# Kernel tuning notes

Hardware: AMD Instinct MI355X
Metric: run time of the kernel (lower is better)

## Reference

```python
import jax, jax.numpy as jnp
import numpy as np

PI = 3.1415927410125732
N = 4096
L = 1.28e-3          # box side [m]
VEL = 5e-7
RC = 3.15e-6         # Rc = diameter/2
RR = 8e-6
RO = 2.5e-5
RA = np.inf
DT_TRANS = 1.4e-14   # DT (translational diffusion)
DR = 0.0028
GAMMA = 25.0
DT = 0.2             # timestep dt
COLL_ITERS = 30      # fixed cap for collision-resolution do-while (orig caps at 1000)


def setup_inputs() -> dict:
    key = jax.random.key(0)
    ks = jax.random.split(key, 7)
    pos_re = jax.random.uniform(ks[0], (N,), jnp.float32) * L
    pos_im = jax.random.uniform(ks[1], (N,), jnp.float32) * L
    ang = jax.random.uniform(ks[2], (N,), jnp.float32, -PI, PI)
    ori_re = jnp.cos(ang)
    ori_im = jnp.sin(ang)
    deltas = jax.random.uniform(ks[3], (N,), jnp.float32) * 0.5
    rot_noise = jax.random.normal(ks[4], (N,), jnp.float32)
    tn_re = jax.random.normal(ks[5], (N,), jnp.float32)
    tn_im = jax.random.normal(ks[6], (N,), jnp.float32)
    return {"pos_re": pos_re, "pos_im": pos_im, "ori_re": ori_re, "ori_im": ori_im,
            "deltas": deltas, "rot_noise": rot_noise, "tn_re": tn_re, "tn_im": tn_im}


def _wrap(diff):
    # torch get_anglediff wrap: (-2pi,2pi) -> ~(-pi,pi)
    diff = jnp.where(diff <= -PI, jnp.mod(diff, PI), diff)
    return diff - (diff >= PI).astype(diff.dtype) * (2.0 * PI)


def _anglediff(a, b):
    return _wrap(jnp.angle(a) - jnp.angle(b))


def _cossim(a, b):
    # nn.CosineSimilarity(dim=1, eps=1e-14) on view_as_real vectors
    dot = a.real * b.real + a.imag * b.imag
    na = jnp.maximum(jnp.abs(a), 1e-14)
    nb = jnp.maximum(jnp.abs(b), 1e-14)
    return dot / (na * nb)


def _mvc(W, z):
    # real [n,n] mask @ complex [n] vector
    return W @ z.real + 1j * (W @ z.imag)


def _solve_collisions(pos):
    n = pos.shape[0]
    eye_f = jnp.eye(n, dtype=jnp.float32)
    eye_c = eye_f.astype(pos.dtype)

    def step(p):
        diff = p[None, :] - p[:, None] + eye_c  # [i,j] = pos_j - pos_i; diag dummy 1 (nan-safe)
        absd = jnp.abs(diff)
        coll = absd <= (2.0 * RC - eye_f)       # diag threshold negative -> self excluded
        move = jnp.where(coll, diff / jnp.where(coll, absd, 1.0) * ((2.1 * RC - absd) * 0.5), 0.0)
        return p - move.sum(axis=1), coll.sum()

    def body(carry, _):
        p, cont = carry
        p_new, ncoll = step(p)
        p = jnp.where(cont, p_new, p)           # do-while: apply move, then continue if collisions
        return (p, jnp.logical_and(cont, ncoll > 0)), None

    body = jax.checkpoint(body)
    (pos, _), _ = jax.lax.scan(body, (pos, jnp.array(True)), None, length=COLL_ITERS)
    return pos


def _forward(pos_re, pos_im, ori_re, ori_im, deltas, rot_noise, tn_re, tn_im):
    pos = (pos_re + 1j * pos_im).astype(jnp.complex64)
    ori = (ori_re + 1j * ori_im).astype(jnp.complex64)
    n = pos.shape[0]
    eye_b = jnp.eye(n, dtype=bool)

    # pairwise |pos_i - pos_j|; diag made 1 to keep abs() grad-safe (diag is masked out / re-added below)
    dists = jnp.abs(pos[:, None] - pos[None, :] + jnp.eye(n, dtype=pos.dtype))
    mask_rr = (dists <= RR) & ~eye_b              # repulsion zone, self excluded (eye subtracted in orig)
    mask_ro = (dists <= RO + RC) | eye_b          # orientation zone, self included (diag dist 0 in orig)
    mask_ra = (dists <= RA + RC) | eye_b          # Ra = inf -> all ones

    # alpha == 2*pi exactly -> within_view branch skipped (matches original)
    ang = jnp.angle(ori)
    abs_ad = jnp.abs(_wrap(ang[:, None] - ang[None, :]))
    in_front = abs_ad < PI / 2

    Wrr = (mask_rr & in_front).astype(jnp.float32)
    Wro = mask_ro.astype(jnp.float32)
    Wra = mask_ra.astype(jnp.float32)

    n_r = Wrr.sum(axis=1)
    S = _mvc(Wrr, pos) / jnp.maximum(n_r, 1.0) - pos * jnp.sign(n_r)
    d = -S

    n_a = Wra.sum(axis=1)
    cms = _mvc(Wra, pos) / jnp.maximum(n_a, 1.0)
    Ps = cms - pos * jnp.sign(n_a)

    osum = _mvc(Wro, ori)
    left = Ps * jnp.exp(1j * deltas)
    right = Ps * jnp.exp(-1j * deltas)

    # T (=300) >= T_release (=200): choose best turn by cosine similarity
    best = jnp.where(_cossim(left, osum) >= _cossim(right, osum), left, right)

    has_rep = jnp.abs(d) > 0.0
    d_safe = jnp.where(has_rep, d, jnp.ones_like(d))
    att = jnp.where(has_rep, _anglediff(d_safe, ori), _anglediff(best, ori))

    s2dr = np.float32(np.sqrt(2.0 * DR))
    sdt = np.float32(np.sqrt(DT))
    rot = jnp.exp(1j * (DT * GAMMA * DR * jnp.sin(att) + rot_noise * s2dr * sdt))

    # complex standard normal: real/imag each N(0, 1/sqrt(2))
    tnoise = (tn_re + 1j * tn_im) * np.float32(np.sqrt(0.5)) * np.float32(np.sqrt(2.0 * DT_TRANS))
    trans = DT * VEL * ori + tnoise * sdt

    new_pos = _solve_collisions(pos + trans)
    new_ori = ori * rot

    c2r = lambda z: jnp.stack([z.real, z.imag], axis=-1)
    # [5, N, 2]: positions, orientations, orientation_sums, leftturns, rightturns (real views)
    return jnp.stack([c2r(new_pos), c2r(new_ori), c2r(osum), c2r(left), c2r(right)], axis=0)


def reference(pos_re, pos_im, ori_re, ori_im, deltas, rot_noise, tn_re, tn_im):
    return _forward(pos_re, pos_im, ori_re, ori_im, deltas, rot_noise, tn_re, tn_im)
```

## Files before the change

### kernel.cpp

```cpp
#include <hip/hip_runtime.h>

#define NPART 4096
#define PI_F 3.1415927410125732f
#define TWO_PI_F 6.2831854820251465f
#define NBCAP 14336
#define SENT 4096

__device__ __forceinline__ float wrapf(float d) {
    if (d <= -PI_F) {
        d = fmodf(d, PI_F);
        if (d < 0.0f) d += PI_F;
    }
    if (d >= PI_F) d -= TWO_PI_F;
    return d;
}

__global__ __launch_bounds__(512)
void k_interact(const float* __restrict__ pr, const float* __restrict__ pim,
                const float* __restrict__ orr, const float* __restrict__ oim,
                const float* __restrict__ deltas,
                const float* __restrict__ rot_noise,
                const float* __restrict__ tn_re, const float* __restrict__ tn_im,
                float* __restrict__ out,
                float2* __restrict__ recPos, int* __restrict__ recMeta,
                unsigned short* __restrict__ recNbr, int* __restrict__ gcnt) {
    constexpr float RR_F  = 8e-6f;
    constexpr float RR2   = RR_F * RR_F;
    constexpr float ROC_F = (float)(2.5e-5 + 3.15e-6);
    constexpr float ROC2  = ROC_F * ROC_F;
    constexpr float CUT_F = 14.3e-6f;
    constexpr float CUT2  = CUT_F * CUT_F;

    __shared__ float4 ls4[512];
    __shared__ float red0[512], red1[512], red2[512], red3[512], red4[512];
    __shared__ float cr_[512], ci_[512];
    __shared__ int ncnt[8];
    __shared__ unsigned short nbrL[8 * 16];

    int tid = threadIdx.x;
    int li = tid & 7, sl = tid >> 3;
    int i = blockIdx.x * 8 + li;

    if (tid < 8) ncnt[tid] = 0;

    float px = pr[i], py = pim[i];
    float ox = orr[i], oy = oim[i];

    float n_r = 0.0f, S_re = 0.0f, S_im = 0.0f, o_re = 0.0f, o_im = 0.0f;
    float cs_re = 0.0f, cs_im = 0.0f;

    for (int c = 0; c < 8; ++c) {
        int j0 = c * 512;
        __syncthreads();
        float jr = pr[j0 + tid], ji = pim[j0 + tid];
        ls4[tid] = make_float4(jr, ji, orr[j0 + tid], oim[j0 + tid]);
        cs_re += jr; cs_im += ji;
        __syncthreads();
#pragma unroll
        for (int t = 0; t < 8; ++t) {
            int jj = sl * 8 + ((t + sl) & 7);
            int j = j0 + jj;
            float4 v = ls4[jj];
            float dr = px - v.x;
            float di = py - v.y;
            float d2 = dr * dr + di * di;
            bool wro = d2 <= ROC2;
            float dot = ox * v.z + oy * v.w;
            bool wrr = (d2 <= RR2) & (dot > 0.0f) & (j != i);
            if (wro) { o_re += v.z; o_im += v.w; }
            if (wrr) { n_r += 1.0f; S_re += v.x; S_im += v.y; }
            if (d2 <= CUT2 && j != i) {
                int slot = atomicAdd(&ncnt[li], 1);
                if (slot < 16) nbrL[li * 16 + slot] = (unsigned short)j;
            }
        }
    }

    red0[tid] = n_r; red1[tid] = S_re; red2[tid] = S_im;
    red3[tid] = o_re; red4[tid] = o_im;
    cr_[tid] = cs_re; ci_[tid] = cs_im;
    __syncthreads();
    for (int s = 256; s > 0; s >>= 1) {
        if (tid < s) { cr_[tid] += cr_[tid + s]; ci_[tid] += ci_[tid + s]; }
        __syncthreads();
    }

    if (tid < 8) {
        for (int s = 1; s < 64; ++s) {
            int t2 = (s << 3) | tid;
            n_r += red0[t2]; S_re += red1[t2]; S_im += red2[t2];
            o_re += red3[t2]; o_im += red4[t2];
        }

        float maxnr = fmaxf(n_r, 1.0f);
        float sgn = (n_r > 0.0f) ? 1.0f : 0.0f;
        float Sre = S_re / maxnr - px * sgn;
        float Sim = S_im / maxnr - py * sgn;
        float d_re = -Sre, d_im = -Sim;

        float cmsx = cr_[0] * (1.0f / 4096.0f);
        float cmsy = ci_[0] * (1.0f / 4096.0f);
        float Ps_re = cmsx - px;
        float Ps_im = cmsy - py;

        float dl = deltas[i];
        float cd = cosf(dl), sd = sinf(dl);
        float l_re = Ps_re * cd - Ps_im * sd;
        float l_im = Ps_re * sd + Ps_im * cd;
        float r_re = Ps_re * cd + Ps_im * sd;
        float r_im = Ps_im * cd - Ps_re * sd;

        float nb   = fmaxf(hypotf(o_re, o_im), 1e-14f);
        float na_l = fmaxf(hypotf(l_re, l_im), 1e-14f);
        float na_r = fmaxf(hypotf(r_re, r_im), 1e-14f);
        float csl = (l_re * o_re + l_im * o_im) / (na_l * nb);
        float csr = (r_re * o_re + r_im * o_im) / (na_r * nb);
        float b_re = (csl >= csr) ? l_re : r_re;
        float b_im = (csl >= csr) ? l_im : r_im;

        float ai = atan2f(oy, ox);
        bool has_rep = (d_re != 0.0f) || (d_im != 0.0f);
        float att;
        if (has_rep) att = wrapf(atan2f(d_im, d_re) - ai);
        else         att = wrapf(atan2f(b_im, b_re) - ai);

        constexpr float GDD  = (float)(0.2 * 25.0 * 0.0028);
        constexpr float S2DR = 0.07483314773547883f;
        constexpr float SDT  = 0.44721359549995793f;
        float theta = GDD * sinf(att) + (rot_noise[i] * S2DR) * SDT;
        float rr_ = cosf(theta), ri_ = sinf(theta);

        float no_re = ox * rr_ - oy * ri_;
        float no_im = ox * ri_ + oy * rr_;

        constexpr float DTVEL = (float)(0.2 * 5e-7);
        constexpr float C1 = 0.70710678118654752f;
        constexpr float C2 = 1.6733200530681511e-07f;
        float t_re = DTVEL * ox + ((tn_re[i] * C1) * C2) * SDT;
        float t_im = DTVEL * oy + ((tn_im[i] * C1) * C2) * SDT;
        float p0x = px + t_re, p0y = py + t_im;

        float2* o2 = (float2*)out;
        o2[i]            = make_float2(p0x, p0y);
        o2[1 * 4096 + i] = make_float2(no_re, no_im);
        o2[2 * 4096 + i] = make_float2(o_re, o_im);
        o2[3 * 4096 + i] = make_float2(l_re, l_im);
        o2[4 * 4096 + i] = make_float2(r_re, r_im);

        int c = min(ncnt[tid], 16);
        if (c > 0) {
            int cp = (c + 3) & ~3;
            int slot = atomicAdd(&gcnt[0], 1);
            int eoff = atomicAdd(&gcnt[1], cp);
            if (eoff + cp <= NBCAP) {
                recPos[slot] = make_float2(p0x, p0y);
                recMeta[slot] = i | (c << 12) | (eoff << 17);
                for (int m = 0; m < cp; ++m)
                    recNbr[eoff + m] = (m < c) ? nbrL[tid * 16 + m]
                                               : (unsigned short)SENT;
            } else {
                recPos[slot] = make_float2(p0x, p0y);
                recMeta[slot] = i;
            }
        }
    }
}

__global__ __launch_bounds__(512)
void k_coll_all(const float2* __restrict__ recPos, const int* __restrict__ recMeta,
                const unsigned short* __restrict__ recNbr,
                const int* __restrict__ gcnt, float* __restrict__ out) {
    constexpr float TWO_RC  = (float)(2.0 * 3.15e-6);
    constexpr float TWO_RC2 = TWO_RC * TWO_RC;
    constexpr float C21RC   = (float)(2.1 * 3.15e-6);

    __shared__ float2 pos[NPART + 2];
    __shared__ unsigned short nbr[NBCAP];
    __shared__ int flg[2];

    int tid = threadIdx.x;
    int n = gcnt[0];
    int totE = min(gcnt[1], NBCAP);

    int nU = (totE + 1) >> 1;
    const unsigned int* src = (const unsigned int*)recNbr;
    unsigned int* dst = (unsigned int*)nbr;
    for (int e = tid; e < nU; e += 512) dst[e] = src[e];

    if (tid == 0) {
        pos[SENT] = make_float2(1e9f, 1e9f);
        flg[0] = 0; flg[1] = 0;
    }

    float myx[8], myy[8];
    int myi[8], myc[8], myo[8];
#pragma unroll
    for (int s = 0; s < 8; ++s) {
        int slot = s * 512 + tid;
        myc[s] = 0; myi[s] = SENT; myo[s] = 0;
        if (slot < n) {
            float2 p = recPos[slot];
            int meta = recMeta[slot];
            myx[s] = p.x; myy[s] = p.y;
            myi[s] = meta & 4095;
            myc[s] = (meta >> 12) & 31;
            myo[s] = (unsigned)meta >> 17;
            pos[myi[s]] = p;
        }
    }
    __syncthreads();

    for (int it = 0; it < 30; ++it) {
        int nc = 0;
        float nx[8], ny[8];
#pragma unroll
        for (int s = 0; s < 8; ++s) {
            int c = myc[s];
            if (c > 0) {
                float px = myx[s], py = myy[s];
                float mre = 0.0f, mim = 0.0f;
                int off = myo[s];
                for (int m0 = 0; m0 < c; m0 += 4) {
                    uint2 w = *(const uint2*)&nbr[off + m0];
                    int j0 = w.x & 0xffff, j1 = w.x >> 16;
                    int j2 = w.y & 0xffff, j3 = w.y >> 16;
                    float2 q0 = pos[j0], q1 = pos[j1], q2 = pos[j2], q3 = pos[j3];
#define COLL_ONE(q)                                                     \
                    {                                                   \
                        float dr = (q).x - px, di = (q).y - py;         \
                        float d2 = dr * dr + di * di;                   \
                        if (d2 <= TWO_RC2) {                            \
                            float a = sqrtf(d2);                        \
                            float mm = (C21RC - a) * 0.5f / a;          \
                            mre += dr * mm; mim += di * mm; ++nc;       \
                        }                                               \
                    }
                    COLL_ONE(q0) COLL_ONE(q1) COLL_ONE(q2) COLL_ONE(q3)
#undef COLL_ONE
                }
                nx[s] = px - mre; ny[s] = py - mim;
            }
        }
        __syncthreads();
#pragma unroll
        for (int s = 0; s < 8; ++s) {
            if (myc[s] > 0) {
                myx[s] = nx[s]; myy[s] = ny[s];
                pos[myi[s]] = make_float2(nx[s], ny[s]);
            }
        }
        if (nc) flg[it & 1] = 1;
        if (tid == 0) flg[(it + 1) & 1] = 0;
        __syncthreads();
        if (flg[it & 1] == 0) break;
    }

    float2* o2 = (float2*)out;
#pragma unroll
    for (int s = 0; s < 8; ++s)
        if (s * 512 + tid < n) o2[myi[s]] = make_float2(myx[s], myy[s]);
}

extern "C" void kernel_launch(void* const* d_in, const int* in_sizes, int n_in,
                              void* d_out, int out_size, void* d_ws, size_t ws_size,
                              hipStream_t stream) {
    const float* pos_re = (const float*)d_in[0];
    const float* pos_im = (const float*)d_in[1];
    const float* ori_re = (const float*)d_in[2];
    const float* ori_im = (const float*)d_in[3];
    const float* deltas = (const float*)d_in[4];
    const float* rot_noise = (const float*)d_in[5];
    const float* tn_re = (const float*)d_in[6];
    const float* tn_im = (const float*)d_in[7];
    float* out = (float*)d_out;

    int* gcnt = (int*)d_ws;
    float2* recPos = (float2*)((char*)d_ws + 16);
    int* recMeta   = (int*)(recPos + NPART);
    unsigned short* recNbr = (unsigned short*)(recMeta + NPART);

    hipMemsetAsync(gcnt, 0, 16, stream);
    k_interact<<<512, 512, 0, stream>>>(pos_re, pos_im, ori_re, ori_im,
                                        deltas, rot_noise, tn_re, tn_im,
                                        out, recPos, recMeta, recNbr, gcnt);
    k_coll_all<<<1, 512, 0, stream>>>(recPos, recMeta, recNbr, gcnt, out);
}
```

Measured before the change: 140.4 us.

## Skip far pairs per wavefront, tree-reduce partials, cache first neighbor quad

```diff
diff --git a/kernel.cpp b/kernel.cpp
--- a/kernel.cpp
+++ b/kernel.cpp
@@ -64,14 +64,16 @@
             float dr = px - v.x;
             float di = py - v.y;
             float d2 = dr * dr + di * di;
-            bool wro = d2 <= ROC2;
-            float dot = ox * v.z + oy * v.w;
-            bool wrr = (d2 <= RR2) & (dot > 0.0f) & (j != i);
-            if (wro) { o_re += v.z; o_im += v.w; }
-            if (wrr) { n_r += 1.0f; S_re += v.x; S_im += v.y; }
-            if (d2 <= CUT2 && j != i) {
-                int slot = atomicAdd(&ncnt[li], 1);
-                if (slot < 16) nbrL[li * 16 + slot] = (unsigned short)j;
+            if (__any(d2 <= ROC2)) {
+                bool wro = d2 <= ROC2;
+                float dot = ox * v.z + oy * v.w;
+                bool wrr = (d2 <= RR2) & (dot > 0.0f) & (j != i);
+                if (wro) { o_re += v.z; o_im += v.w; }
+                if (wrr) { n_r += 1.0f; S_re += v.x; S_im += v.y; }
+                if (d2 <= CUT2 && j != i) {
+                    int slot = atomicAdd(&ncnt[li], 1);
+                    if (slot < 16) nbrL[li * 16 + slot] = (unsigned short)j;
+                }
             }
         }
     }
@@ -80,17 +82,25 @@
     red3[tid] = o_re; red4[tid] = o_im;
     cr_[tid] = cs_re; ci_[tid] = cs_im;
     __syncthreads();
-    for (int s = 256; s > 0; s >>= 1) {
-        if (tid < s) { cr_[tid] += cr_[tid + s]; ci_[tid] += ci_[tid + s]; }
-        __syncthreads();
-    }
+    for (int s = 256; s >= 8; s >>= 1) {
+        if (tid < s) {
+            red0[tid] += red0[tid + s]; red1[tid] += red1[tid + s];
+            red2[tid] += red2[tid + s]; red3[tid] += red3[tid + s];
+            red4[tid] += red4[tid + s];
+            cr_[tid] += cr_[tid + s];  ci_[tid] += ci_[tid + s];
+        }
+        __syncthreads();
+    }
+    if (tid < 4) { cr_[tid] += cr_[tid + 4]; ci_[tid] += ci_[tid + 4]; }
+    __syncthreads();
+    if (tid < 2) { cr_[tid] += cr_[tid + 2]; ci_[tid] += ci_[tid + 2]; }
+    __syncthreads();
+    if (tid == 0) { cr_[0] += cr_[1]; ci_[0] += ci_[1]; }
+    __syncthreads();
 
     if (tid < 8) {
-        for (int s = 1; s < 64; ++s) {
-            int t2 = (s << 3) | tid;
-            n_r += red0[t2]; S_re += red1[t2]; S_im += red2[t2];
-            o_re += red3[t2]; o_im += red4[t2];
-        }
+        n_r = red0[tid]; S_re = red1[tid]; S_im = red2[tid];
+        o_re = red3[tid]; o_im = red4[tid];
 
         float maxnr = fmaxf(n_r, 1.0f);
         float sgn = (n_r > 0.0f) ? 1.0f : 0.0f;
@@ -175,17 +185,17 @@
     constexpr float C21RC   = (float)(2.1 * 3.15e-6);
 
     __shared__ float2 pos[NPART + 2];
-    __shared__ unsigned short nbr[NBCAP];
+    __shared__ __align__(16) unsigned short nbr[NBCAP];
     __shared__ int flg[2];
 
     int tid = threadIdx.x;
     int n = gcnt[0];
     int totE = min(gcnt[1], NBCAP);
 
-    int nU = (totE + 1) >> 1;
-    const unsigned int* src = (const unsigned int*)recNbr;
-    unsigned int* dst = (unsigned int*)nbr;
-    for (int e = tid; e < nU; e += 512) dst[e] = src[e];
+    int nU4 = (totE + 7) >> 3;
+    const uint4* src4 = (const uint4*)recNbr;
+    uint4* dst4 = (uint4*)nbr;
+    for (int e = tid; e < nU4; e += 512) dst4[e] = src4[e];
 
     if (tid == 0) {
         pos[SENT] = make_float2(1e9f, 1e9f);
@@ -210,34 +220,50 @@
     }
     __syncthreads();
 
+    int nq0[8], nq1[8], nq2[8], nq3[8];
+#pragma unroll
+    for (int s = 0; s < 8; ++s) {
+        nq0[s] = SENT; nq1[s] = SENT; nq2[s] = SENT; nq3[s] = SENT;
+        if (myc[s] > 0) {
+            uint2 w = *(const uint2*)&nbr[myo[s]];
+            nq0[s] = w.x & 0xffff; nq1[s] = w.x >> 16;
+            nq2[s] = w.y & 0xffff; nq3[s] = w.y >> 16;
+        }
+    }
+
     for (int it = 0; it < 30; ++it) {
-        int nc = 0;
         float nx[8], ny[8];
+        int ncs[8];
 #pragma unroll
         for (int s = 0; s < 8; ++s) {
+            ncs[s] = 0;
             int c = myc[s];
             if (c > 0) {
                 float px = myx[s], py = myy[s];
                 float mre = 0.0f, mim = 0.0f;
-                int off = myo[s];
-                for (int m0 = 0; m0 < c; m0 += 4) {
-                    uint2 w = *(const uint2*)&nbr[off + m0];
+                int nc = 0;
+                float2 q0 = pos[nq0[s]], q1 = pos[nq1[s]];
+                float2 q2 = pos[nq2[s]], q3 = pos[nq3[s]];
+#define COLL_ONE(q)                                                     \
+                {                                                       \
+                    float dr = (q).x - px, di = (q).y - py;             \
+                    float d2 = dr * dr + di * di;                       \
+                    if (d2 <= TWO_RC2) {                                \
+                        float a = sqrtf(d2);                            \
+                        float mm = (C21RC - a) * 0.5f / a;              \
+                        mre += dr * mm; mim += di * mm; ++nc;           \
+                    }                                                   \
+                }
+                COLL_ONE(q0) COLL_ONE(q1) COLL_ONE(q2) COLL_ONE(q3)
+                for (int m0 = 4; m0 < c; m0 += 4) {
+                    uint2 w = *(const uint2*)&nbr[myo[s] + m0];
                     int j0 = w.x & 0xffff, j1 = w.x >> 16;
                     int j2 = w.y & 0xffff, j3 = w.y >> 16;
-                    float2 q0 = pos[j0], q1 = pos[j1], q2 = pos[j2], q3 = pos[j3];
-#define COLL_ONE(q)                                                     \
-                    {                                                   \
-                        float dr = (q).x - px, di = (q).y - py;         \
-                        float d2 = dr * dr + di * di;                   \
-                        if (d2 <= TWO_RC2) {                            \
-                            float a = sqrtf(d2);                        \
-                            float mm = (C21RC - a) * 0.5f / a;          \
-                            mre += dr * mm; mim += di * mm; ++nc;       \
-                        }                                               \
-                    }
-                    COLL_ONE(q0) COLL_ONE(q1) COLL_ONE(q2) COLL_ONE(q3)
+                    float2 t0 = pos[j0], t1 = pos[j1], t2 = pos[j2], t3 = pos[j3];
+                    COLL_ONE(t0) COLL_ONE(t1) COLL_ONE(t2) COLL_ONE(t3)
+                }
 #undef COLL_ONE
-                }
+                ncs[s] = nc;
                 nx[s] = px - mre; ny[s] = py - mim;
             }
         }
@@ -249,7 +275,9 @@
                 pos[myi[s]] = make_float2(nx[s], ny[s]);
             }
         }
-        if (nc) flg[it & 1] = 1;
+        int any = ncs[0] | ncs[1] | ncs[2] | ncs[3] |
+                  ncs[4] | ncs[5] | ncs[6] | ncs[7];
+        if (any) flg[it & 1] = 1;
         if (tid == 0) flg[(it + 1) & 1] = 0;
         __syncthreads();
         if (flg[it & 1] == 0) break;
```

Result: faster. 130.1 us (-7.3%).
